# Kernel optimization log

Hardware: AMD Instinct MI355X
Metric: run time of the kernel (lower is better)

The kernel has to match this reference:

```python
import jax, jax.numpy as jnp
import numpy as np

NUM_LAYERS = 4
N_EDGE_TYPES = 3
RBAR = 1
DIM = 128
N_NODES = 50000
N_EDGES = 600000
N_HOP_LAYERS = NUM_LAYERS * (NUM_LAYERS + 1) // 2  # 10
EPS = 1e-12


def setup_inputs() -> dict:
    key = jax.random.key(0)
    ks = jax.random.split(key, 8)
    x = jax.random.normal(ks[0], (N_NODES, DIM), dtype=jnp.float32)
    edge_index = jax.random.randint(ks[1], (2, N_EDGES), 0, N_NODES, dtype=jnp.int64)
    edge_hop = jax.random.randint(ks[2], (N_EDGES,), 0, NUM_LAYERS + 1, dtype=jnp.int64)
    edge_type = jax.random.randint(ks[3], (N_EDGES,), 0, N_EDGE_TYPES, dtype=jnp.int64)
    scale = 1.0 / np.sqrt(DIM)
    W_edge = jax.random.normal(ks[4], (N_EDGE_TYPES, DIM, DIM), dtype=jnp.float32) * scale
    b_edge = jnp.zeros((N_EDGE_TYPES, DIM), dtype=jnp.float32)
    W_hop = jax.random.normal(ks[5], (N_HOP_LAYERS, DIM, DIM), dtype=jnp.float32) * scale
    b_hop = jnp.zeros((N_HOP_LAYERS, DIM), dtype=jnp.float32)
    return {"x": x, "edge_index": edge_index, "edge_hop": edge_hop,
            "edge_type": edge_type, "W_edge": W_edge, "b_edge": b_edge,
            "W_hop": W_hop, "b_hop": b_hop}


def _conv(h_in, W, b, src, dst, mask, n_nodes):
    """GraphConv sub-layer on a masked edge subset: sum_{j->i, mask} (x_j W) + b."""
    h = h_in @ W                                  # [N, d]
    msg = h[src] * mask[:, None]                  # [E, d], masked gather
    agg = jax.ops.segment_sum(msg, dst, num_segments=n_nodes)
    return agg + b


def reference(x, edge_index, edge_hop, edge_type, W_edge, b_edge, W_hop, b_hop):
    n_nodes = x.shape[0]
    src, dst = edge_index[0], edge_index[1]
    xs = []
    cur = x
    idx = 0  # sequential consumption of hop sub-layers (next(modules))
    for t in range(NUM_LAYERS):
        xs.append(cur)
        acc = jnp.zeros_like(cur)
        # relation-specific sub-layers, always on x[t]
        for e in range(N_EDGE_TYPES):
            mask = (edge_type == e).astype(cur.dtype)
            acc = acc + _conv(xs[t], W_edge[e], b_edge[e], src, dst, mask, n_nodes)
        # delay / k-hop sub-layers, k = 1..t+1, reading delayed state x[t-delay]
        for k in range(1, t + 2):
            delay = max(k - RBAR, 0)
            mask = (edge_hop == k).astype(cur.dtype)
            acc = acc + _conv(xs[t - delay], W_hop[idx], b_hop[idx], src, dst, mask, n_nodes)
            idx += 1
        cur = xs[t] + jax.nn.relu(acc)
        # F.normalize(p=2, dim=-1): x / max(||x||_2, eps)
        norm = jnp.linalg.norm(cur, axis=-1, keepdims=True)
        cur = cur / jnp.maximum(norm, EPS)
    return cur
```

## Files before the change

kernel.cpp:

```cpp
#include <hip/hip_runtime.h>
#include <hip/hip_bf16.h>

#define DIM 128
#define NLAYER 4

typedef _Float16 f16x8 __attribute__((ext_vector_type(8)));
typedef _Float16 f16x2 __attribute__((ext_vector_type(2)));
typedef float f32x4 __attribute__((ext_vector_type(4)));


__global__ void k_count(const int* __restrict__ dst, int E, int* __restrict__ counts) {
    int e = blockIdx.x * blockDim.x + threadIdx.x;
    if (e < E) atomicAdd(&counts[dst[e]], 1);
}

__global__ __launch_bounds__(1024) void k_scan1(const int* __restrict__ in, int n,
                                                int* __restrict__ partial,
                                                int* __restrict__ blockSums) {
    __shared__ int sd[1024];
    int tid = threadIdx.x;
    int i = blockIdx.x * 1024 + tid;
    int v = (i < n) ? in[i] : 0;
    sd[tid] = v;
    __syncthreads();
    for (int off = 1; off < 1024; off <<= 1) {
        int t = (tid >= off) ? sd[tid - off] : 0;
        __syncthreads();
        sd[tid] += t;
        __syncthreads();
    }
    if (i < n) partial[i] = sd[tid];
    if (tid == 1023) blockSums[blockIdx.x] = sd[1023];
}

__global__ void k_scan2(int* __restrict__ bs, int nb) {
    int lane = threadIdx.x;
    int v = (lane < nb) ? bs[lane] : 0;
    for (int off = 1; off < 64; off <<= 1) {
        int t = __shfl_up(v, off, 64);
        if (lane >= off) v += t;
    }
    int ex = __shfl_up(v, 1, 64);
    if (lane == 0) ex = 0;
    if (lane < nb) bs[lane] = ex;
}

__global__ __launch_bounds__(1024) void k_scan3(const int* __restrict__ partial,
                                                const int* __restrict__ bs, int n,
                                                int* __restrict__ row_ptr,
                                                int* __restrict__ cursor) {
    int i = blockIdx.x * blockDim.x + threadIdx.x;
    if (i < n) {
        int v = partial[i] + bs[i >> 10];
        row_ptr[i + 1] = v;
        cursor[i + 1] = v;
    }
    if (i == 0) { row_ptr[0] = 0; cursor[0] = 0; }
}

__global__ void k_scatter(const int* __restrict__ srcA, const int* __restrict__ dstA,
                          const int* __restrict__ typA, const int* __restrict__ hopA,
                          int E, int* __restrict__ cursor, unsigned* __restrict__ csr) {
    int e = blockIdx.x * blockDim.x + threadIdx.x;
    if (e < E) {
        int d = dstA[e];
        int p = atomicAdd(&cursor[d], 1);
        csr[p] = ((unsigned)srcA[e] << 8) | ((unsigned)typA[e] << 24)
               | ((unsigned)hopA[e] << 26);
    }
}

__global__ void k_bias(const float* __restrict__ b_edge, const float* __restrict__ b_hop,
                       float* __restrict__ bias_sums) {
    int t = blockIdx.x, d = threadIdx.x;
    float s = b_edge[d] + b_edge[DIM + d] + b_edge[2 * DIM + d];
    int base = t * (t + 1) / 2;
    for (int k = 1; k <= t + 1; ++k) s += b_hop[(base + k - 1) * DIM + d];
    bias_sums[t * DIM + d] = s;
}


__global__ void k_convX(const float* __restrict__ in, _Float16* __restrict__ out, int n) {
    int i = (blockIdx.x * blockDim.x + threadIdx.x) * 8;
    if (i >= n) return;
    float4 a = ((const float4*)(in + i))[0];
    float4 b = ((const float4*)(in + i))[1];
    f16x8 o;
    o[0] = (_Float16)a.x; o[1] = (_Float16)a.y; o[2] = (_Float16)a.z; o[3] = (_Float16)a.w;
    o[4] = (_Float16)b.x; o[5] = (_Float16)b.y; o[6] = (_Float16)b.z; o[7] = (_Float16)b.w;
    *(f16x8*)(out + i) = o;
}

__global__ __launch_bounds__(256) void k_convW(const float* __restrict__ W_edge,
                                               const float* __restrict__ W_hop,
                                               _Float16* __restrict__ Wt) {
    int s = blockIdx.x;
    const float* src = (s < 3) ? (W_edge + (size_t)s * DIM * DIM)
                               : (W_hop + (size_t)(s - 3) * DIM * DIM);
    _Float16* dstp = Wt + (size_t)s * DIM * DIM;
    for (int it = 0; it < 64; ++it) {
        int e = it * 256 + threadIdx.x;
        int n = e >> 7, k = e & 127;
        dstp[e] = (_Float16)src[k * DIM + n];
    }
}


struct GatherArgs {
    const _Float16* xt;
    _Float16* Atype;
    _Float16* Ahop;
    const int* row_ptr;
    const unsigned* csr;
    int N;
};

template <int TAU>
__global__ __launch_bounds__(256) void k_gather(GatherArgs a) {
    const int wid = threadIdx.x >> 6, lane = threadIdx.x & 63;
    const int node = blockIdx.x * 4 + wid;
    if (node >= a.N) return;
    const size_t NS = (size_t)a.N * DIM;

    const char* xtl = (const char*)a.xt + lane * 4;

    float t0x = 0, t0y = 0, t1x = 0, t1y = 0, t2x = 0, t2y = 0;
    float h1x = 0, h1y = 0, h2x = 0, h2y = 0, h3x = 0, h3y = 0, h4x = 0, h4y = 0;

    const int e0 = a.row_ptr[node], e1 = a.row_ptr[node + 1];
    int e = e0;

    #define ACCUM(m, v)                                                        \
        {                                                                      \
            const int typ = (int)((m) >> 24) & 3;                              \
            const int hop = (int)((m) >> 26);                                  \
            const float vx = (float)(v)[0], vy = (float)(v)[1];                \
            if (typ == 0)      { t0x += vx; t0y += vy; }                       \
            else if (typ == 1) { t1x += vx; t1y += vy; }                       \
            else               { t2x += vx; t2y += vy; }                       \
            if (hop == 1)                    { h1x += vx; h1y += vy; }         \
            else if (TAU <= 2 && hop == 2)   { h2x += vx; h2y += vy; }         \
            else if (TAU <= 1 && hop == 3)   { h3x += vx; h3y += vy; }         \
            else if (TAU == 0 && hop == 4)   { h4x += vx; h4y += vy; }         \
        }

    for (; e + 8 <= e1; e += 8) {
        unsigned mm[8];
        #pragma unroll
        for (int j = 0; j < 8; ++j) mm[j] = a.csr[e + j];
        f16x2 vv[8];
        #pragma unroll
        for (int j = 0; j < 8; ++j)
            vv[j] = *(const f16x2*)(xtl + (mm[j] & 0xFFFFFF));
        #pragma unroll
        for (int j = 0; j < 8; ++j) ACCUM(mm[j], vv[j])
    }
    for (; e + 4 <= e1; e += 4) {
        unsigned mm[4];
        #pragma unroll
        for (int j = 0; j < 4; ++j) mm[j] = a.csr[e + j];
        f16x2 vv[4];
        #pragma unroll
        for (int j = 0; j < 4; ++j)
            vv[j] = *(const f16x2*)(xtl + (mm[j] & 0xFFFFFF));
        #pragma unroll
        for (int j = 0; j < 4; ++j) ACCUM(mm[j], vv[j])
    }
    for (; e < e1; ++e) {
        const unsigned m = a.csr[e];
        const f16x2 v = *(const f16x2*)(xtl + (m & 0xFFFFFF));
        ACCUM(m, v)
    }
    #undef ACCUM

    _Float16* tb = a.Atype + (size_t)node * DIM;
    f16x2 o;
    o[0] = (_Float16)t0x; o[1] = (_Float16)t0y; ((f16x2*)(tb + 0 * NS))[lane] = o;
    o[0] = (_Float16)t1x; o[1] = (_Float16)t1y; ((f16x2*)(tb + 1 * NS))[lane] = o;
    o[0] = (_Float16)t2x; o[1] = (_Float16)t2y; ((f16x2*)(tb + 2 * NS))[lane] = o;

    _Float16* hb = a.Ahop + (size_t)node * DIM;
    constexpr int i1 = (TAU * (TAU + 1)) / 2;
    o[0] = (_Float16)h1x; o[1] = (_Float16)h1y; ((f16x2*)(hb + (size_t)i1 * NS))[lane] = o;
    if (TAU <= 2) {
        constexpr int tp = TAU + 1;
        constexpr int i2 = (tp * (tp + 1)) / 2 + 1;
        o[0] = (_Float16)h2x; o[1] = (_Float16)h2y; ((f16x2*)(hb + (size_t)i2 * NS))[lane] = o;
    }
    if (TAU <= 1) {
        constexpr int tp = TAU + 2;
        constexpr int i3 = (tp * (tp + 1)) / 2 + 2;
        o[0] = (_Float16)h3x; o[1] = (_Float16)h3y; ((f16x2*)(hb + (size_t)i3 * NS))[lane] = o;
    }
    if (TAU == 0) {
        constexpr int i4 = (3 * 4) / 2 + 3;
        o[0] = (_Float16)h4x; o[1] = (_Float16)h4y; ((f16x2*)(hb + (size_t)i4 * NS))[lane] = o;
    }
}


struct GemmArgs {
    const _Float16* Aslot[7];
    const _Float16* Wt;
    const _Float16* xin;
    const float* bias;
    float* outf;
    _Float16* outh;
    int N;
    int wsel[7];
};

template <int NSUB>
__global__ __launch_bounds__(128, 2) void k_gemm(GemmArgs a) {
    __shared__ __align__(16) _Float16 Wlds[DIM * DIM];
    const int tid = threadIdx.x, wv = tid >> 6, lane = tid & 63;
    const int rowBase = blockIdx.x * 64 + wv * 32;
    const int lr = lane & 15, lg = lane >> 4;

    int r0 = rowBase + lr, r1 = rowBase + 16 + lr;
    if (r0 >= a.N) r0 = a.N - 1;
    if (r1 >= a.N) r1 = a.N - 1;

    f32x4 acc[2][8];
    #pragma unroll
    for (int rt = 0; rt < 2; ++rt)
        #pragma unroll
        for (int ct = 0; ct < 8; ++ct)
            acc[rt][ct] = (f32x4){0.f, 0.f, 0.f, 0.f};

    const int sw = (lr & 7) << 4;

    {
        const _Float16* Ws = a.Wt + (size_t)a.wsel[0] * (DIM * DIM);
        f16x8 w[16];
        #pragma unroll
        for (int i = 0; i < 16; ++i)
            w[i] = *(const f16x8*)((const char*)Ws + i * 2048 + tid * 16);
        #pragma unroll
        for (int i = 0; i < 16; ++i) {
            const int p = i * 2048 + tid * 16;
            const int q = p ^ (((p >> 8) & 7) << 4);
            *(f16x8*)((char*)Wlds + q) = w[i];
        }
    }
    f16x8 afA[2][4], afB[2][4];
    #pragma unroll
    for (int ks = 0; ks < 4; ++ks) {
        afA[0][ks] = *(const f16x8*)(a.Aslot[0] + (size_t)r0 * DIM + ks * 32 + lg * 8);
        afB[0][ks] = *(const f16x8*)(a.Aslot[0] + (size_t)r1 * DIM + ks * 32 + lg * 8);
    }
    __syncthreads();

    #pragma unroll
    for (int s = 0; s < NSUB; ++s) {
        const int cur = s & 1, nxt = cur ^ 1;
        f16x8 w[16];
        if (s + 1 < NSUB) {
            const _Float16* Wn = a.Wt + (size_t)a.wsel[s + 1] * (DIM * DIM);
            #pragma unroll
            for (int i = 0; i < 16; ++i)
                w[i] = *(const f16x8*)((const char*)Wn + i * 2048 + tid * 16);
            const _Float16* An = a.Aslot[s + 1];
            #pragma unroll
            for (int ks = 0; ks < 4; ++ks) {
                afA[nxt][ks] = *(const f16x8*)(An + (size_t)r0 * DIM + ks * 32 + lg * 8);
                afB[nxt][ks] = *(const f16x8*)(An + (size_t)r1 * DIM + ks * 32 + lg * 8);
            }
        }
        #pragma unroll
        for (int ks = 0; ks < 4; ++ks) {
            const int cb = (ks * 32 + lg * 8) * 2;
            #pragma unroll
            for (int ct = 0; ct < 8; ++ct) {
                const int addr = (ct * 16 + lr) * 256 + (cb ^ sw);
                const f16x8 bf = *(const f16x8*)((const char*)Wlds + addr);
                acc[0][ct] = __builtin_amdgcn_mfma_f32_16x16x32_f16(afA[cur][ks], bf, acc[0][ct], 0, 0, 0);
                acc[1][ct] = __builtin_amdgcn_mfma_f32_16x16x32_f16(afB[cur][ks], bf, acc[1][ct], 0, 0, 0);
            }
        }
        __syncthreads();
        if (s + 1 < NSUB) {
            #pragma unroll
            for (int i = 0; i < 16; ++i) {
                const int p = i * 2048 + tid * 16;
                const int q = p ^ (((p >> 8) & 7) << 4);
                *(f16x8*)((char*)Wlds + q) = w[i];
            }
            __syncthreads();
        }
    }

    float bv[8];
    #pragma unroll
    for (int ct = 0; ct < 8; ++ct) bv[ct] = a.bias[ct * 16 + lr];

    #pragma unroll
    for (int rt = 0; rt < 2; ++rt) {
        #pragma unroll
        for (int rg = 0; rg < 4; ++rg) {
            const int row = rowBase + rt * 16 + lg * 4 + rg;
            const int rr = (row < a.N) ? row : a.N - 1;
            float v[8];
            float ss = 0.f;
            #pragma unroll
            for (int ct = 0; ct < 8; ++ct) {
                const float xval = (float)a.xin[(size_t)rr * DIM + ct * 16 + lr];
                const float tv = fmaxf(acc[rt][ct][rg] + bv[ct], 0.f) + xval;
                v[ct] = tv;
                ss += tv * tv;
            }
            ss += __shfl_xor(ss, 1, 64);
            ss += __shfl_xor(ss, 2, 64);
            ss += __shfl_xor(ss, 4, 64);
            ss += __shfl_xor(ss, 8, 64);
            const float inv = 1.f / fmaxf(sqrtf(ss), 1e-12f);
            if (row < a.N) {
                #pragma unroll
                for (int ct = 0; ct < 8; ++ct) {
                    const int col = ct * 16 + lr;
                    const float ov = v[ct] * inv;
                    if (a.outf) a.outf[(size_t)row * DIM + col] = ov;
                    if (a.outh) a.outh[(size_t)row * DIM + col] = (_Float16)ov;
                }
            }
        }
    }
}


static inline size_t align_up(size_t v, size_t a) { return (v + a - 1) & ~(a - 1); }

extern "C" void kernel_launch(void* const* d_in, const int* in_sizes, int n_in,
                              void* d_out, int out_size, void* d_ws, size_t ws_size,
                              hipStream_t stream) {
    const float* x        = (const float*)d_in[0];
    const int* edge_index = (const int*)d_in[1];
    const int* edge_hop   = (const int*)d_in[2];
    const int* edge_type  = (const int*)d_in[3];
    const float* W_edge   = (const float*)d_in[4];
    const float* b_edge   = (const float*)d_in[5];
    const float* W_hop    = (const float*)d_in[6];
    const float* b_hop    = (const float*)d_in[7];
    float* out = (float*)d_out;

    int N = in_sizes[0] / DIM;
    int E = in_sizes[2];
    const int* srcA = edge_index;
    const int* dstA = edge_index + E;

    size_t NSh = (size_t)N * DIM * sizeof(_Float16);
    size_t off = 0;
    char* wsb = (char*)d_ws;
    _Float16* xh0     = (_Float16*)(wsb + off);  off = align_up(off + NSh, 64);
    _Float16* xh1     = (_Float16*)(wsb + off);  off = align_up(off + NSh, 64);
    _Float16* xh2     = (_Float16*)(wsb + off);  off = align_up(off + NSh, 64);
    _Float16* xh3     = (_Float16*)(wsb + off);  off = align_up(off + NSh, 64);
    _Float16* Atype   = (_Float16*)(wsb + off);  off = align_up(off + 3 * NSh, 64);
    _Float16* Ahop    = (_Float16*)(wsb + off);  off = align_up(off + 10 * NSh, 64);
    _Float16* Wt      = (_Float16*)(wsb + off);  off = align_up(off + 13 * DIM * DIM * sizeof(_Float16), 64);
    int* counts       = (int*)(wsb + off);       off = align_up(off + (size_t)N * 4, 64);
    int* partial      = (int*)(wsb + off);       off = align_up(off + (size_t)N * 4, 64);
    int* blockSums    = (int*)(wsb + off);       off = align_up(off + 64 * 4, 64);
    int* row_ptr      = (int*)(wsb + off);       off = align_up(off + (size_t)(N + 1) * 4, 64);
    int* cursor       = (int*)(wsb + off);       off = align_up(off + (size_t)(N + 1) * 4, 64);
    unsigned* csr     = (unsigned*)(wsb + off);  off = align_up(off + (size_t)E * 4, 64);
    float* bias_sums  = (float*)(wsb + off);     off = align_up(off + 4 * DIM * 4, 64);
    (void)ws_size;

    hipMemsetAsync(counts, 0, (size_t)N * 4, stream);
    k_count<<<(E + 255) / 256, 256, 0, stream>>>(dstA, E, counts);
    int nb = (N + 1023) / 1024;
    k_scan1<<<nb, 1024, 0, stream>>>(counts, N, partial, blockSums);
    k_scan2<<<1, 64, 0, stream>>>(blockSums, nb);
    k_scan3<<<nb, 1024, 0, stream>>>(partial, blockSums, N, row_ptr, cursor);
    k_scatter<<<(E + 255) / 256, 256, 0, stream>>>(srcA, dstA, edge_type, edge_hop, E, cursor, csr);
    k_bias<<<4, DIM, 0, stream>>>(b_edge, b_hop, bias_sums);

    k_convX<<<(N * DIM / 8 + 255) / 256, 256, 0, stream>>>(x, xh0, N * DIM);
    k_convW<<<13, 256, 0, stream>>>(W_edge, W_hop, Wt);

    _Float16* xh_ptr[4] = { xh0, xh1, xh2, xh3 };
    const size_t NS = (size_t)N * DIM;

    for (int t = 0; t < NLAYER; ++t) {
        GatherArgs g;
        g.xt = xh_ptr[t];
        g.Atype = Atype; g.Ahop = Ahop;
        g.row_ptr = row_ptr; g.csr = csr; g.N = N;
        const int gbg = (N + 3) / 4;
        switch (t) {
            case 0: k_gather<0><<<gbg, 256, 0, stream>>>(g); break;
            case 1: k_gather<1><<<gbg, 256, 0, stream>>>(g); break;
            case 2: k_gather<2><<<gbg, 256, 0, stream>>>(g); break;
            default: k_gather<3><<<gbg, 256, 0, stream>>>(g); break;
        }

        GemmArgs m;
        m.Wt = Wt; m.xin = xh_ptr[t];
        m.bias = bias_sums + t * DIM;
        m.outf = (t == 3) ? out : nullptr;
        m.outh = (t < 3) ? xh_ptr[t + 1] : nullptr;
        m.N = N;
        const int nsub = t + 4;
        const int base = t * (t + 1) / 2;
        for (int s = 0; s < 3; ++s) { m.wsel[s] = s; m.Aslot[s] = Atype + (size_t)s * NS; }
        for (int j = 0; j <= t; ++j) {
            m.wsel[3 + j] = 3 + base + j;
            m.Aslot[3 + j] = Ahop + (size_t)(base + j) * NS;
        }
        for (int s = nsub; s < 7; ++s) { m.wsel[s] = 0; m.Aslot[s] = Atype; }

        const int gb = (N + 63) / 64;
        switch (nsub) {
            case 4: k_gemm<4><<<gb, 128, 0, stream>>>(m); break;
            case 5: k_gemm<5><<<gb, 128, 0, stream>>>(m); break;
            case 6: k_gemm<6><<<gb, 128, 0, stream>>>(m); break;
            default: k_gemm<7><<<gb, 128, 0, stream>>>(m); break;
        }
    }
}
```

Before: 353.0 us.

## Alias hop aggregate buffers, use one-wave gather blocks, add restrict qualifiers

Hop aggregation slots whose lifetimes do not overlap now share physical buffers through a PHYS mapping, shrinking the Ahop workspace from ten slots to seven. The gather kernel launches one 64-thread block per node instead of four wavefronts per block, and its argument pointers gain __restrict__. The intent is a smaller working set with better cache locality and finer-grained scheduling. The cost is more, smaller blocks and a correctness dependence on the slot lifetimes in the mapping.

```diff
diff --git a/kernel.cpp b/kernel.cpp
--- a/kernel.cpp
+++ b/kernel.cpp
@@ -7,6 +7,8 @@
 typedef _Float16 f16x8 __attribute__((ext_vector_type(8)));
 typedef _Float16 f16x2 __attribute__((ext_vector_type(2)));
 typedef float f32x4 __attribute__((ext_vector_type(4)));
+
+static constexpr int PHYS[10] = {0, 4, 1, 0, 5, 2, 1, 4, 6, 3};
 
 
 __global__ void k_count(const int* __restrict__ dst, int E, int* __restrict__ counts) {
@@ -107,19 +109,18 @@
 
 
 struct GatherArgs {
-    const _Float16* xt;
-    _Float16* Atype;
-    _Float16* Ahop;
-    const int* row_ptr;
-    const unsigned* csr;
+    const _Float16* __restrict__ xt;
+    _Float16* __restrict__ Atype;
+    _Float16* __restrict__ Ahop;
+    const int* __restrict__ row_ptr;
+    const unsigned* __restrict__ csr;
     int N;
 };
 
 template <int TAU>
-__global__ __launch_bounds__(256) void k_gather(GatherArgs a) {
-    const int wid = threadIdx.x >> 6, lane = threadIdx.x & 63;
-    const int node = blockIdx.x * 4 + wid;
-    if (node >= a.N) return;
+__global__ __launch_bounds__(64) void k_gather(GatherArgs a) {
+    const int node = blockIdx.x;
+    const int lane = threadIdx.x;
     const size_t NS = (size_t)a.N * DIM;
 
     const char* xtl = (const char*)a.xt + lane * 4;
@@ -180,21 +181,21 @@
     o[0] = (_Float16)t2x; o[1] = (_Float16)t2y; ((f16x2*)(tb + 2 * NS))[lane] = o;
 
     _Float16* hb = a.Ahop + (size_t)node * DIM;
-    constexpr int i1 = (TAU * (TAU + 1)) / 2;
-    o[0] = (_Float16)h1x; o[1] = (_Float16)h1y; ((f16x2*)(hb + (size_t)i1 * NS))[lane] = o;
-    if (TAU <= 2) {
-        constexpr int tp = TAU + 1;
-        constexpr int i2 = (tp * (tp + 1)) / 2 + 1;
-        o[0] = (_Float16)h2x; o[1] = (_Float16)h2y; ((f16x2*)(hb + (size_t)i2 * NS))[lane] = o;
-    }
-    if (TAU <= 1) {
-        constexpr int tp = TAU + 2;
-        constexpr int i3 = (tp * (tp + 1)) / 2 + 2;
-        o[0] = (_Float16)h3x; o[1] = (_Float16)h3y; ((f16x2*)(hb + (size_t)i3 * NS))[lane] = o;
-    }
-    if (TAU == 0) {
-        constexpr int i4 = (3 * 4) / 2 + 3;
-        o[0] = (_Float16)h4x; o[1] = (_Float16)h4y; ((f16x2*)(hb + (size_t)i4 * NS))[lane] = o;
+    {
+        constexpr int P1 = PHYS[(TAU * (TAU + 1)) / 2];
+        o[0] = (_Float16)h1x; o[1] = (_Float16)h1y; ((f16x2*)(hb + (size_t)P1 * NS))[lane] = o;
+    }
+    if constexpr (TAU <= 2) {
+        constexpr int P2 = PHYS[((TAU + 1) * (TAU + 2)) / 2 + 1];
+        o[0] = (_Float16)h2x; o[1] = (_Float16)h2y; ((f16x2*)(hb + (size_t)P2 * NS))[lane] = o;
+    }
+    if constexpr (TAU <= 1) {
+        constexpr int P3 = PHYS[((TAU + 2) * (TAU + 3)) / 2 + 2];
+        o[0] = (_Float16)h3x; o[1] = (_Float16)h3y; ((f16x2*)(hb + (size_t)P3 * NS))[lane] = o;
+    }
+    if constexpr (TAU == 0) {
+        constexpr int P4 = PHYS[9];
+        o[0] = (_Float16)h4x; o[1] = (_Float16)h4y; ((f16x2*)(hb + (size_t)P4 * NS))[lane] = o;
     }
 }
 
@@ -356,7 +357,7 @@
     _Float16* xh2     = (_Float16*)(wsb + off);  off = align_up(off + NSh, 64);
     _Float16* xh3     = (_Float16*)(wsb + off);  off = align_up(off + NSh, 64);
     _Float16* Atype   = (_Float16*)(wsb + off);  off = align_up(off + 3 * NSh, 64);
-    _Float16* Ahop    = (_Float16*)(wsb + off);  off = align_up(off + 10 * NSh, 64);
+    _Float16* Ahop    = (_Float16*)(wsb + off);  off = align_up(off + 7 * NSh, 64);
     _Float16* Wt      = (_Float16*)(wsb + off);  off = align_up(off + 13 * DIM * DIM * sizeof(_Float16), 64);
     int* counts       = (int*)(wsb + off);       off = align_up(off + (size_t)N * 4, 64);
     int* partial      = (int*)(wsb + off);       off = align_up(off + (size_t)N * 4, 64);
@@ -387,12 +388,11 @@
         g.xt = xh_ptr[t];
         g.Atype = Atype; g.Ahop = Ahop;
         g.row_ptr = row_ptr; g.csr = csr; g.N = N;
-        const int gbg = (N + 3) / 4;
         switch (t) {
-            case 0: k_gather<0><<<gbg, 256, 0, stream>>>(g); break;
-            case 1: k_gather<1><<<gbg, 256, 0, stream>>>(g); break;
-            case 2: k_gather<2><<<gbg, 256, 0, stream>>>(g); break;
-            default: k_gather<3><<<gbg, 256, 0, stream>>>(g); break;
+            case 0: k_gather<0><<<N, 64, 0, stream>>>(g); break;
+            case 1: k_gather<1><<<N, 64, 0, stream>>>(g); break;
+            case 2: k_gather<2><<<N, 64, 0, stream>>>(g); break;
+            default: k_gather<3><<<N, 64, 0, stream>>>(g); break;
         }
 
         GemmArgs m;
@@ -406,7 +406,7 @@
         for (int s = 0; s < 3; ++s) { m.wsel[s] = s; m.Aslot[s] = Atype + (size_t)s * NS; }
         for (int j = 0; j <= t; ++j) {
             m.wsel[3 + j] = 3 + base + j;
-            m.Aslot[3 + j] = Ahop + (size_t)(base + j) * NS;
+            m.Aslot[3 + j] = Ahop + (size_t)PHYS[base + j] * NS;
         }
         for (int s = nsub; s < 7; ++s) { m.wsel[s] = 0; m.Aslot[s] = Atype; }
 
```

New measurement: 343.6 us. -2.7%, faster.
